# Kernel optimization log

Measured on AMD Instinct MI355X. Metric: run time of the kernel, lower is better.

The kernel has to match this reference:

```python
import jax, jax.numpy as jnp
import numpy as np

NUM_STEPS = 10
T0, T1 = 0.0, 1.0


def setup_inputs() -> dict:
    key = jax.random.key(0)
    ks = jax.random.split(key, 6)
    B, I, H = 4096, 1024, 2048
    sc_ih = 1.0 / np.sqrt(I)
    sc_hh = 1.0 / np.sqrt(H)
    return {
        "x": jax.random.normal(ks[0], (B, I), jnp.float32),
        "h0": jax.random.normal(ks[1], (B, H), jnp.float32),
        "W_ih": jax.random.normal(ks[2], (H, I), jnp.float32) * sc_ih,
        "b_ih": jax.random.normal(ks[3], (H,), jnp.float32) * sc_ih,
        "W_hh": jax.random.normal(ks[4], (H, H), jnp.float32) * sc_hh,
        "b_hh": jax.random.normal(ks[5], (H,), jnp.float32) * sc_hh,
        "tau": jnp.ones((H,), jnp.float32),
    }


def reference(x, h0, W_ih, b_ih, W_hh, b_hh, tau):
    dt = (T1 - T0) / NUM_STEPS
    # time-invariant input drive: W_ih(input) is the same every step
    ih = x @ W_ih.T + b_ih  # [B, H]
    decay = jnp.exp(-dt / tau)  # [H]

    def step(h, _):
        pre = ih + h @ W_hh.T + b_hh
        target = jnp.tanh(pre)
        h_new = decay * h + (1.0 - decay) * target
        return h_new, None

    h_final, _ = jax.lax.scan(step, h0, None, length=NUM_STEPS)
    return h_final
```

## Files before the change

### kernel.cpp

```cpp
#include <hip/hip_runtime.h>
#include <hip/hip_bf16.h>

#define NUM_STEPS 10
#define DT 0.1f

typedef __bf16 bf16_t;
typedef __bf16 bf16x8 __attribute__((ext_vector_type(8)));
typedef __bf16 bf16x4 __attribute__((ext_vector_type(4)));
typedef float f32x4 __attribute__((ext_vector_type(4)));

__device__ __forceinline__ void async16(const bf16_t* g, bf16_t* l) {
  __builtin_amdgcn_global_load_lds(
      (const __attribute__((address_space(1))) void*)g,
      (__attribute__((address_space(3))) void*)l, 16, 0, 0);
}

__global__ void cvt_f32_to_bf16(const float* __restrict__ in,
                                bf16_t* __restrict__ out, int n4) {
  int i = blockIdx.x * blockDim.x + threadIdx.x;
  if (i < n4) {
    float4 v = ((const float4*)in)[i];
    bf16x4 o = {(bf16_t)v.x, (bf16_t)v.y, (bf16_t)v.z, (bf16_t)v.w};
    ((bf16x4*)out)[i] = o;
  }
}

__global__ void make_decay(const float* __restrict__ tau,
                           float* __restrict__ decay, int n) {
  int i = blockIdx.x * blockDim.x + threadIdx.x;
  if (i < n) decay[i] = __expf(-DT / tau[i]);
}

template <int EPI>
__global__ __launch_bounds__(512, 2) void gemm_nt(
    const bf16_t* __restrict__ A, const bf16_t* __restrict__ Bw, int M, int N,
    int K, const float* __restrict__ bias1, const float* __restrict__ bias2,
    bf16_t* __restrict__ out_ihb, const bf16_t* __restrict__ ihb,
    const float* __restrict__ decay, const bf16_t* __restrict__ hb_prev,
    bf16_t* __restrict__ hb_next, float* __restrict__ out_f32, int writeOut) {
  extern __shared__ char smem[];

  const int tid = threadIdx.x;
  const int lane = tid & 63;
  const int wave = tid >> 6;
  const int waveM = wave >> 1;
  const int waveN = wave & 1;

  const int lin = blockIdx.y * gridDim.x + blockIdx.x;
  const int xcd = lin & 7;
  const int slot = lin >> 3;
  const int bx = (xcd & 1) * 8 + (slot & 7);
  const int by = (xcd >> 1) * 4 + (slot >> 3);
  const long bRow = (long)by * 256;
  const long bCol = (long)bx * 128;

  const int laneRow = lane & 15;
  const int laneK = (lane >> 4) << 3;
  const bf16_t* aG0 = A + (bRow + (wave * 2 + 0) * 16 + laneRow) * (long)K + laneK;
  const bf16_t* aG1 = A + (bRow + (wave * 2 + 1) * 16 + laneRow) * (long)K + laneK;
  const bf16_t* bG = Bw + (bCol + wave * 16 + laneRow) * (long)K + laneK;

  f32x4 acc[4][4] = {};

  auto stage = [&](int buf, int k0) {
    bf16_t* base = (bf16_t*)(smem + buf * 49152);
    async16(aG0 + k0, base + (wave * 2 + 0) * 1024);
    async16(aG0 + k0 + 32, base + (wave * 2 + 0) * 1024 + 512);
    async16(aG1 + k0, base + (wave * 2 + 1) * 1024);
    async16(aG1 + k0 + 32, base + (wave * 2 + 1) * 1024 + 512);
    async16(bG + k0, base + 16384 + wave * 1024);
    async16(bG + k0 + 32, base + 16384 + wave * 1024 + 512);
  };

  auto compute = [&](int buf) {
    const bf16_t* Ab = (const bf16_t*)(smem + buf * 49152);
    const bf16_t* Bb = Ab + 16384;
#pragma unroll
    for (int ks = 0; ks < 2; ++ks) {
      bf16x8 aF[4], bF[4];
#pragma unroll
      for (int t = 0; t < 4; ++t)
        aF[t] = *(const bf16x8*)&Ab[(waveM * 4 + t) * 1024 + ks * 512 + lane * 8];
#pragma unroll
      for (int u = 0; u < 4; ++u)
        bF[u] = *(const bf16x8*)&Bb[(waveN * 4 + u) * 1024 + ks * 512 + lane * 8];
      __builtin_amdgcn_s_setprio(1);
#pragma unroll
      for (int t = 0; t < 4; ++t)
#pragma unroll
        for (int u = 0; u < 4; ++u)
          acc[t][u] = __builtin_amdgcn_mfma_f32_16x16x32_bf16(aF[t], bF[u],
                                                              acc[t][u], 0, 0, 0);
      __builtin_amdgcn_s_setprio(0);
    }
  };

  const int NT = K >> 6;

  stage(0, 0);
  stage(1, 64);
  asm volatile("s_waitcnt vmcnt(6)" ::: "memory");
  __builtin_amdgcn_s_barrier();
  __builtin_amdgcn_sched_barrier(0);

  int cb = 0, sb = 2;
  for (int t = 0; t < NT - 2; ++t) {
    stage(sb, (t + 2) * 64);
    __builtin_amdgcn_sched_barrier(0);
    compute(cb);
    asm volatile("s_waitcnt lgkmcnt(0)" ::: "memory");
    asm volatile("s_waitcnt vmcnt(6)" ::: "memory");
    __builtin_amdgcn_s_barrier();
    __builtin_amdgcn_sched_barrier(0);
    cb = cb + 1; if (cb == 3) cb = 0;
    sb = sb + 1; if (sb == 3) sb = 0;
  }
  compute(cb);
  asm volatile("s_waitcnt lgkmcnt(0)" ::: "memory");
  asm volatile("s_waitcnt vmcnt(0)" ::: "memory");
  __builtin_amdgcn_s_barrier();
  __builtin_amdgcn_sched_barrier(0);
  cb = cb + 1; if (cb == 3) cb = 0;
  compute(cb);
  asm volatile("s_waitcnt lgkmcnt(0)" ::: "memory");
  __builtin_amdgcn_s_barrier();
  __builtin_amdgcn_sched_barrier(0);

  float* Ep = (float*)smem;
  const int eRow = (lane >> 4) << 2;
  const int eCol = lane & 15;
#pragma unroll
  for (int t = 0; t < 4; ++t)
#pragma unroll
    for (int u = 0; u < 4; ++u)
#pragma unroll
      for (int r = 0; r < 4; ++r) {
        const int rowL = waveM * 64 + t * 16 + eRow + r;
        const int colL = waveN * 64 + u * 16 + eCol;
        Ep[rowL * 128 + ((colL + 4 * rowL) & 127)] = acc[t][u][r];
      }
  asm volatile("s_waitcnt lgkmcnt(0)" ::: "memory");
  __builtin_amdgcn_s_barrier();
  __builtin_amdgcn_sched_barrier(0);

  const int rdRow = tid >> 3;
  const int col0 = (tid & 7) * 16;
#pragma unroll
  for (int p = 0; p < 4; ++p) {
    const int row = p * 64 + rdRow;
    float v[16];
#pragma unroll
    for (int c = 0; c < 4; ++c)
      *(f32x4*)&v[c * 4] =
          *(const f32x4*)&Ep[row * 128 + ((col0 + 4 * c + 4 * row) & 127)];
    const long g = (bRow + row) * (long)N + bCol + col0;

    if (EPI == 0) {
      f32x4 b1[4], b2[4];
#pragma unroll
      for (int c = 0; c < 4; ++c) {
        b1[c] = *(const f32x4*)&bias1[bCol + col0 + c * 4];
        b2[c] = *(const f32x4*)&bias2[bCol + col0 + c * 4];
      }
      bf16x8 o0, o1;
#pragma unroll
      for (int e = 0; e < 8; ++e)
        o0[e] = (bf16_t)(v[e] + b1[e >> 2][e & 3] + b2[e >> 2][e & 3]);
#pragma unroll
      for (int e = 0; e < 8; ++e)
        o1[e] = (bf16_t)(v[8 + e] + b1[2 + (e >> 2)][e & 3] +
                         b2[2 + (e >> 2)][e & 3]);
      *(bf16x8*)&out_ihb[g] = o0;
      *(bf16x8*)&out_ihb[g + 8] = o1;
    } else {
      const bf16x8 ih0 = *(const bf16x8*)&ihb[g];
      const bf16x8 ih1 = *(const bf16x8*)&ihb[g + 8];
      const bf16x8 hp0 = *(const bf16x8*)&hb_prev[g];
      const bf16x8 hp1 = *(const bf16x8*)&hb_prev[g + 8];
      f32x4 dc[4];
#pragma unroll
      for (int c = 0; c < 4; ++c)
        dc[c] = *(const f32x4*)&decay[bCol + col0 + c * 4];
      float hn[16];
      bf16x8 o0, o1;
#pragma unroll
      for (int e = 0; e < 8; ++e) {
        const float d = dc[e >> 2][e & 3];
        const float th = tanhf(v[e] + (float)ih0[e]);
        hn[e] = d * (float)hp0[e] + (1.0f - d) * th;
        o0[e] = (bf16_t)hn[e];
      }
#pragma unroll
      for (int e = 0; e < 8; ++e) {
        const float d = dc[2 + (e >> 2)][e & 3];
        const float th = tanhf(v[8 + e] + (float)ih1[e]);
        hn[8 + e] = d * (float)hp1[e] + (1.0f - d) * th;
        o1[e] = (bf16_t)hn[8 + e];
      }
      *(bf16x8*)&hb_next[g] = o0;
      *(bf16x8*)&hb_next[g + 8] = o1;
      if (writeOut) {
#pragma unroll
        for (int c = 0; c < 4; ++c)
          *(f32x4*)&out_f32[g + c * 4] = *(const f32x4*)&hn[c * 4];
      }
    }
  }
}

extern "C" void kernel_launch(void* const* d_in, const int* in_sizes, int n_in,
                              void* d_out, int out_size, void* d_ws,
                              size_t ws_size, hipStream_t stream) {
  const float* x = (const float*)d_in[0];
  const float* h0 = (const float*)d_in[1];
  const float* W_ih = (const float*)d_in[2];
  const float* b_ih = (const float*)d_in[3];
  const float* W_hh = (const float*)d_in[4];
  const float* b_hh = (const float*)d_in[5];
  const float* tau = (const float*)d_in[6];
  float* hout = (float*)d_out;

  const int B = 4096, I = 1024, H = 2048;

  char* ws = (char*)d_ws;
  bf16_t* ihb = (bf16_t*)ws; ws += (size_t)B * H * 2;
  bf16_t* hb0 = (bf16_t*)ws; ws += (size_t)B * H * 2;
  bf16_t* hb1 = (bf16_t*)ws; ws += (size_t)B * H * 2;
  bf16_t* xb = (bf16_t*)ws;  ws += (size_t)B * I * 2;
  bf16_t* wihb = (bf16_t*)ws; ws += (size_t)H * I * 2;
  bf16_t* whhb = (bf16_t*)ws; ws += (size_t)H * H * 2;
  float* decay = (float*)ws; ws += (size_t)H * 4;

  const int LDS_BYTES = 147456;
  (void)hipFuncSetAttribute(reinterpret_cast<const void*>(&gemm_nt<0>),
                            hipFuncAttributeMaxDynamicSharedMemorySize,
                            LDS_BYTES);
  (void)hipFuncSetAttribute(reinterpret_cast<const void*>(&gemm_nt<1>),
                            hipFuncAttributeMaxDynamicSharedMemorySize,
                            LDS_BYTES);

  cvt_f32_to_bf16<<<(B * I / 4 + 255) / 256, 256, 0, stream>>>(x, xb, B * I / 4);
  cvt_f32_to_bf16<<<(H * I / 4 + 255) / 256, 256, 0, stream>>>(W_ih, wihb, H * I / 4);
  cvt_f32_to_bf16<<<(H * H / 4 + 255) / 256, 256, 0, stream>>>(W_hh, whhb, H * H / 4);
  cvt_f32_to_bf16<<<(B * H / 4 + 255) / 256, 256, 0, stream>>>(h0, hb0, B * H / 4);
  make_decay<<<(H + 255) / 256, 256, 0, stream>>>(tau, decay, H);

  dim3 grid(H / 128, B / 256);
  gemm_nt<0><<<grid, 512, LDS_BYTES, stream>>>(
      xb, wihb, B, H, I, b_ih, b_hh, ihb, nullptr, nullptr, nullptr, nullptr,
      nullptr, 0);

  bf16_t* hb[2] = {hb0, hb1};
  for (int s = 0; s < NUM_STEPS; ++s) {
    gemm_nt<1><<<grid, 512, LDS_BYTES, stream>>>(
        hb[s & 1], whhb, B, H, H, nullptr, nullptr, nullptr, ihb, decay,
        hb[s & 1], hb[(s + 1) & 1], hout, (s == NUM_STEPS - 1) ? 1 : 0);
  }
}
```

Measured before the change: 735.9 us.

## Replace triple-buffered K pipeline with half-tile staged double buffering

Replaces the three-stage LDS ring with two buffers. Each 64-wide K tile is split into two 32-wide halves that are loaded and computed in alternating phases, so the next tile's halves are prefetched while the current halves are consumed. This shrinks the dynamic LDS request to the size the epilogue needs and aims to overlap global loads with MFMA work at a finer grain. In exchange it adds a second barrier per K tile and leaves less prefetch distance to hide memory latency.

```diff
diff --git a/kernel.cpp b/kernel.cpp
--- a/kernel.cpp
+++ b/kernel.cpp
@@ -62,69 +62,81 @@
 
   f32x4 acc[4][4] = {};
 
-  auto stage = [&](int buf, int k0) {
+  auto stage_h = [&](int buf, int k0, int ks) {
     bf16_t* base = (bf16_t*)(smem + buf * 49152);
-    async16(aG0 + k0, base + (wave * 2 + 0) * 1024);
-    async16(aG0 + k0 + 32, base + (wave * 2 + 0) * 1024 + 512);
-    async16(aG1 + k0, base + (wave * 2 + 1) * 1024);
-    async16(aG1 + k0 + 32, base + (wave * 2 + 1) * 1024 + 512);
-    async16(bG + k0, base + 16384 + wave * 1024);
-    async16(bG + k0 + 32, base + 16384 + wave * 1024 + 512);
+    const int ko = k0 + ks * 32;
+    async16(aG0 + ko, base + (wave * 2 + 0) * 1024 + ks * 512);
+    async16(aG1 + ko, base + (wave * 2 + 1) * 1024 + ks * 512);
+    async16(bG + ko, base + 16384 + wave * 1024 + ks * 512);
   };
 
-  auto compute = [&](int buf) {
+  auto phase_compute = [&](int buf, int ks) {
     const bf16_t* Ab = (const bf16_t*)(smem + buf * 49152);
     const bf16_t* Bb = Ab + 16384;
-#pragma unroll
-    for (int ks = 0; ks < 2; ++ks) {
-      bf16x8 aF[4], bF[4];
-#pragma unroll
-      for (int t = 0; t < 4; ++t)
-        aF[t] = *(const bf16x8*)&Ab[(waveM * 4 + t) * 1024 + ks * 512 + lane * 8];
+    bf16x8 aF[4], bF[4];
+#pragma unroll
+    for (int t = 0; t < 4; ++t)
+      aF[t] = *(const bf16x8*)&Ab[(waveM * 4 + t) * 1024 + ks * 512 + lane * 8];
+#pragma unroll
+    for (int u = 0; u < 4; ++u)
+      bF[u] = *(const bf16x8*)&Bb[(waveN * 4 + u) * 1024 + ks * 512 + lane * 8];
+    __builtin_amdgcn_s_setprio(1);
+#pragma unroll
+    for (int t = 0; t < 4; ++t)
 #pragma unroll
       for (int u = 0; u < 4; ++u)
-        bF[u] = *(const bf16x8*)&Bb[(waveN * 4 + u) * 1024 + ks * 512 + lane * 8];
-      __builtin_amdgcn_s_setprio(1);
-#pragma unroll
-      for (int t = 0; t < 4; ++t)
-#pragma unroll
-        for (int u = 0; u < 4; ++u)
-          acc[t][u] = __builtin_amdgcn_mfma_f32_16x16x32_bf16(aF[t], bF[u],
-                                                              acc[t][u], 0, 0, 0);
-      __builtin_amdgcn_s_setprio(0);
-    }
+        acc[t][u] = __builtin_amdgcn_mfma_f32_16x16x32_bf16(aF[t], bF[u],
+                                                            acc[t][u], 0, 0, 0);
+    __builtin_amdgcn_s_setprio(0);
   };
 
   const int NT = K >> 6;
 
-  stage(0, 0);
-  stage(1, 64);
+  stage_h(0, 0, 0);
+  stage_h(0, 0, 1);
+  stage_h(1, 64, 0);
   asm volatile("s_waitcnt vmcnt(6)" ::: "memory");
   __builtin_amdgcn_s_barrier();
   __builtin_amdgcn_sched_barrier(0);
 
-  int cb = 0, sb = 2;
+  int cur = 0;
   for (int t = 0; t < NT - 2; ++t) {
-    stage(sb, (t + 2) * 64);
-    __builtin_amdgcn_sched_barrier(0);
-    compute(cb);
+    const int k0 = t * 64;
+    stage_h(cur ^ 1, k0 + 64, 1);
+    phase_compute(cur, 0);
+    asm volatile("s_waitcnt vmcnt(6)" ::: "memory");
+    __builtin_amdgcn_s_barrier();
+    __builtin_amdgcn_sched_barrier(0);
+    stage_h(cur, k0 + 128, 0);
+    phase_compute(cur, 1);
+    asm volatile("s_waitcnt vmcnt(6)" ::: "memory");
+    __builtin_amdgcn_s_barrier();
+    __builtin_amdgcn_sched_barrier(0);
+    cur ^= 1;
+  }
+  {
+    const int k0 = (NT - 2) * 64;
+    stage_h(cur ^ 1, k0 + 64, 1);
+    phase_compute(cur, 0);
+    asm volatile("s_waitcnt vmcnt(6)" ::: "memory");
+    __builtin_amdgcn_s_barrier();
+    __builtin_amdgcn_sched_barrier(0);
+    phase_compute(cur, 1);
+    asm volatile("s_waitcnt vmcnt(3)" ::: "memory");
+    __builtin_amdgcn_s_barrier();
+    __builtin_amdgcn_sched_barrier(0);
+    cur ^= 1;
+  }
+  {
+    phase_compute(cur, 0);
+    asm volatile("s_waitcnt vmcnt(0)" ::: "memory");
+    __builtin_amdgcn_s_barrier();
+    __builtin_amdgcn_sched_barrier(0);
+    phase_compute(cur, 1);
     asm volatile("s_waitcnt lgkmcnt(0)" ::: "memory");
-    asm volatile("s_waitcnt vmcnt(6)" ::: "memory");
-    __builtin_amdgcn_s_barrier();
-    __builtin_amdgcn_sched_barrier(0);
-    cb = cb + 1; if (cb == 3) cb = 0;
-    sb = sb + 1; if (sb == 3) sb = 0;
-  }
-  compute(cb);
-  asm volatile("s_waitcnt lgkmcnt(0)" ::: "memory");
-  asm volatile("s_waitcnt vmcnt(0)" ::: "memory");
-  __builtin_amdgcn_s_barrier();
-  __builtin_amdgcn_sched_barrier(0);
-  cb = cb + 1; if (cb == 3) cb = 0;
-  compute(cb);
-  asm volatile("s_waitcnt lgkmcnt(0)" ::: "memory");
-  __builtin_amdgcn_s_barrier();
-  __builtin_amdgcn_sched_barrier(0);
+    __builtin_amdgcn_s_barrier();
+    __builtin_amdgcn_sched_barrier(0);
+  }
 
   float* Ep = (float*)smem;
   const int eRow = (lane >> 4) << 2;
@@ -231,7 +243,7 @@
   bf16_t* whhb = (bf16_t*)ws; ws += (size_t)H * H * 2;
   float* decay = (float*)ws; ws += (size_t)H * 4;
 
-  const int LDS_BYTES = 147456;
+  const int LDS_BYTES = 131072;
   (void)hipFuncSetAttribute(reinterpret_cast<const void*>(&gemm_nt<0>),
                             hipFuncAttributeMaxDynamicSharedMemorySize,
                             LDS_BYTES);
```

Result: no change. 736.7 us (+0.1%).

## Double GEMM block to 16 waves with smaller per-wave tiles

Applied to the files above, without the earlier changes.

Doubles the GEMM workgroup from 8 to 16 waves, so each wave owns a 64x32 output tile (4x2 MFMA accumulators) instead of 64x64, and the async global-to-LDS staging is spread across more waves. The per-k-step compute is split into two calls, and the lgkmcnt wait inside the main loop is removed. The aim is more waves in flight to hide memory latency, with lower register pressure per wave. The cost is smaller per-wave reuse: more LDS fragment reads per MFMA and barriers spanning 16 waves. Only one 1024-thread block fits per CU because of the LDS allocation, so the launch-bounds occupancy hint of 4 is not reachable.

```diff
diff --git a/kernel.cpp b/kernel.cpp
--- a/kernel.cpp
+++ b/kernel.cpp
@@ -32,7 +32,7 @@
 }
 
 template <int EPI>
-__global__ __launch_bounds__(512, 2) void gemm_nt(
+__global__ __launch_bounds__(1024, 4) void gemm_nt(
     const bf16_t* __restrict__ A, const bf16_t* __restrict__ Bw, int M, int N,
     int K, const float* __restrict__ bias1, const float* __restrict__ bias2,
     bf16_t* __restrict__ out_ihb, const bf16_t* __restrict__ ihb,
@@ -43,8 +43,8 @@
   const int tid = threadIdx.x;
   const int lane = tid & 63;
   const int wave = tid >> 6;
-  const int waveM = wave >> 1;
-  const int waveN = wave & 1;
+  const int waveM = wave >> 2;
+  const int waveN = wave & 3;
 
   const int lin = blockIdx.y * gridDim.x + blockIdx.x;
   const int xcd = lin & 7;
@@ -56,50 +56,46 @@
 
   const int laneRow = lane & 15;
   const int laneK = (lane >> 4) << 3;
-  const bf16_t* aG0 = A + (bRow + (wave * 2 + 0) * 16 + laneRow) * (long)K + laneK;
-  const bf16_t* aG1 = A + (bRow + (wave * 2 + 1) * 16 + laneRow) * (long)K + laneK;
-  const bf16_t* bG = Bw + (bCol + wave * 16 + laneRow) * (long)K + laneK;
-
-  f32x4 acc[4][4] = {};
+  const bf16_t* aG = A + (bRow + wave * 16 + laneRow) * (long)K + laneK;
+  const bf16_t* bG = Bw + (bCol + (wave & 7) * 16 + laneRow) * (long)K +
+                     laneK + (wave >> 3) * 32;
+  const int aOff = wave * 1024;
+  const int bOff = 16384 + (wave & 7) * 1024 + (wave >> 3) * 512;
+
+  f32x4 acc[4][2] = {};
 
   auto stage = [&](int buf, int k0) {
     bf16_t* base = (bf16_t*)(smem + buf * 49152);
-    async16(aG0 + k0, base + (wave * 2 + 0) * 1024);
-    async16(aG0 + k0 + 32, base + (wave * 2 + 0) * 1024 + 512);
-    async16(aG1 + k0, base + (wave * 2 + 1) * 1024);
-    async16(aG1 + k0 + 32, base + (wave * 2 + 1) * 1024 + 512);
-    async16(bG + k0, base + 16384 + wave * 1024);
-    async16(bG + k0 + 32, base + 16384 + wave * 1024 + 512);
+    async16(aG + k0, base + aOff);
+    async16(aG + k0 + 32, base + aOff + 512);
+    async16(bG + k0, base + bOff);
   };
 
-  auto compute = [&](int buf) {
+  auto compute = [&](int buf, int ks) {
     const bf16_t* Ab = (const bf16_t*)(smem + buf * 49152);
     const bf16_t* Bb = Ab + 16384;
-#pragma unroll
-    for (int ks = 0; ks < 2; ++ks) {
-      bf16x8 aF[4], bF[4];
-#pragma unroll
-      for (int t = 0; t < 4; ++t)
-        aF[t] = *(const bf16x8*)&Ab[(waveM * 4 + t) * 1024 + ks * 512 + lane * 8];
-#pragma unroll
-      for (int u = 0; u < 4; ++u)
-        bF[u] = *(const bf16x8*)&Bb[(waveN * 4 + u) * 1024 + ks * 512 + lane * 8];
-      __builtin_amdgcn_s_setprio(1);
-#pragma unroll
-      for (int t = 0; t < 4; ++t)
-#pragma unroll
-        for (int u = 0; u < 4; ++u)
-          acc[t][u] = __builtin_amdgcn_mfma_f32_16x16x32_bf16(aF[t], bF[u],
-                                                              acc[t][u], 0, 0, 0);
-      __builtin_amdgcn_s_setprio(0);
-    }
+    bf16x8 aF[4], bF[2];
+#pragma unroll
+    for (int t = 0; t < 4; ++t)
+      aF[t] = *(const bf16x8*)&Ab[(waveM * 4 + t) * 1024 + ks * 512 + lane * 8];
+#pragma unroll
+    for (int u = 0; u < 2; ++u)
+      bF[u] = *(const bf16x8*)&Bb[(waveN * 2 + u) * 1024 + ks * 512 + lane * 8];
+    __builtin_amdgcn_s_setprio(1);
+#pragma unroll
+    for (int t = 0; t < 4; ++t)
+#pragma unroll
+      for (int u = 0; u < 2; ++u)
+        acc[t][u] = __builtin_amdgcn_mfma_f32_16x16x32_bf16(aF[t], bF[u],
+                                                            acc[t][u], 0, 0, 0);
+    __builtin_amdgcn_s_setprio(0);
   };
 
   const int NT = K >> 6;
 
   stage(0, 0);
   stage(1, 64);
-  asm volatile("s_waitcnt vmcnt(6)" ::: "memory");
+  asm volatile("s_waitcnt vmcnt(3)" ::: "memory");
   __builtin_amdgcn_s_barrier();
   __builtin_amdgcn_sched_barrier(0);
 
@@ -107,21 +103,22 @@
   for (int t = 0; t < NT - 2; ++t) {
     stage(sb, (t + 2) * 64);
     __builtin_amdgcn_sched_barrier(0);
-    compute(cb);
-    asm volatile("s_waitcnt lgkmcnt(0)" ::: "memory");
-    asm volatile("s_waitcnt vmcnt(6)" ::: "memory");
+    compute(cb, 0);
+    compute(cb, 1);
+    asm volatile("s_waitcnt vmcnt(3)" ::: "memory");
     __builtin_amdgcn_s_barrier();
     __builtin_amdgcn_sched_barrier(0);
     cb = cb + 1; if (cb == 3) cb = 0;
     sb = sb + 1; if (sb == 3) sb = 0;
   }
-  compute(cb);
-  asm volatile("s_waitcnt lgkmcnt(0)" ::: "memory");
+  compute(cb, 0);
+  compute(cb, 1);
   asm volatile("s_waitcnt vmcnt(0)" ::: "memory");
   __builtin_amdgcn_s_barrier();
   __builtin_amdgcn_sched_barrier(0);
   cb = cb + 1; if (cb == 3) cb = 0;
-  compute(cb);
+  compute(cb, 0);
+  compute(cb, 1);
   asm volatile("s_waitcnt lgkmcnt(0)" ::: "memory");
   __builtin_amdgcn_s_barrier();
   __builtin_amdgcn_sched_barrier(0);
@@ -132,11 +129,11 @@
 #pragma unroll
   for (int t = 0; t < 4; ++t)
 #pragma unroll
-    for (int u = 0; u < 4; ++u)
+    for (int u = 0; u < 2; ++u)
 #pragma unroll
       for (int r = 0; r < 4; ++r) {
         const int rowL = waveM * 64 + t * 16 + eRow + r;
-        const int colL = waveN * 64 + u * 16 + eCol;
+        const int colL = waveN * 32 + u * 16 + eCol;
         Ep[rowL * 128 + ((colL + 4 * rowL) & 127)] = acc[t][u][r];
       }
   asm volatile("s_waitcnt lgkmcnt(0)" ::: "memory");
@@ -146,8 +143,8 @@
   const int rdRow = tid >> 3;
   const int col0 = (tid & 7) * 16;
 #pragma unroll
-  for (int p = 0; p < 4; ++p) {
-    const int row = p * 64 + rdRow;
+  for (int p = 0; p < 2; ++p) {
+    const int row = p * 128 + rdRow;
     float v[16];
 #pragma unroll
     for (int c = 0; c < 4; ++c)
@@ -246,13 +243,13 @@
   make_decay<<<(H + 255) / 256, 256, 0, stream>>>(tau, decay, H);
 
   dim3 grid(H / 128, B / 256);
-  gemm_nt<0><<<grid, 512, LDS_BYTES, stream>>>(
+  gemm_nt<0><<<grid, 1024, LDS_BYTES, stream>>>(
       xb, wihb, B, H, I, b_ih, b_hh, ihb, nullptr, nullptr, nullptr, nullptr,
       nullptr, 0);
 
   bf16_t* hb[2] = {hb0, hb1};
   for (int s = 0; s < NUM_STEPS; ++s) {
-    gemm_nt<1><<<grid, 512, LDS_BYTES, stream>>>(
+    gemm_nt<1><<<grid, 1024, LDS_BYTES, stream>>>(
         hb[s & 1], whhb, B, H, H, nullptr, nullptr, nullptr, ihb, decay,
         hb[s & 1], hb[(s + 1) & 1], hout, (s == NUM_STEPS - 1) ? 1 : 0);
   }
```

New measurement: 729.1 us. No clear change (-0.9%).

## Split k-tile into two half-phases interleaving A/B prefetch with MFMA clusters

Applied to the files above, without the earlier changes.

Restructures the GEMM main loop so each 64-wide k-tile is processed in two 32-wide phases. Each phase issues its LDS fragment reads, then half of the next tile's async global-to-LDS loads (A in one phase, B in the other), then a barrier and its MFMA cluster. The A tile staging layout also changes so each wave loads rows wave and wave+8 (lo/hi halves) instead of two adjacent 16-row blocks. The aim is to spread the global load issue through the loop and overlap it better with compute, at the cost of an extra barrier per tile.

```diff
diff --git a/kernel.cpp b/kernel.cpp
--- a/kernel.cpp
+++ b/kernel.cpp
@@ -3,6 +3,7 @@
 
 #define NUM_STEPS 10
 #define DT 0.1f
+#define SLOT_BYTES 49152
 
 typedef __bf16 bf16_t;
 typedef __bf16 bf16x8 __attribute__((ext_vector_type(8)));
@@ -48,96 +49,114 @@
 
   const int lin = blockIdx.y * gridDim.x + blockIdx.x;
   const int xcd = lin & 7;
-  const int slot = lin >> 3;
-  const int bx = (xcd & 1) * 8 + (slot & 7);
-  const int by = (xcd >> 1) * 4 + (slot >> 3);
+  const int slot_ = lin >> 3;
+  const int bx = (xcd & 1) * 8 + (slot_ & 7);
+  const int by = (xcd >> 1) * 4 + (slot_ >> 3);
   const long bRow = (long)by * 256;
   const long bCol = (long)bx * 128;
 
   const int laneRow = lane & 15;
   const int laneK = (lane >> 4) << 3;
-  const bf16_t* aG0 = A + (bRow + (wave * 2 + 0) * 16 + laneRow) * (long)K + laneK;
-  const bf16_t* aG1 = A + (bRow + (wave * 2 + 1) * 16 + laneRow) * (long)K + laneK;
+  const bf16_t* aGlo = A + (bRow + wave * 16 + laneRow) * (long)K + laneK;
+  const bf16_t* aGhi = A + (bRow + 128 + wave * 16 + laneRow) * (long)K + laneK;
   const bf16_t* bG = Bw + (bCol + wave * 16 + laneRow) * (long)K + laneK;
 
   f32x4 acc[4][4] = {};
 
-  auto stage = [&](int buf, int k0) {
-    bf16_t* base = (bf16_t*)(smem + buf * 49152);
-    async16(aG0 + k0, base + (wave * 2 + 0) * 1024);
-    async16(aG0 + k0 + 32, base + (wave * 2 + 0) * 1024 + 512);
-    async16(aG1 + k0, base + (wave * 2 + 1) * 1024);
-    async16(aG1 + k0 + 32, base + (wave * 2 + 1) * 1024 + 512);
+  auto stageA = [&](int slot, int k0) {
+    bf16_t* base = (bf16_t*)(smem + slot * SLOT_BYTES);
+    async16(aGlo + k0, base + wave * 1024);
+    async16(aGlo + k0 + 32, base + wave * 1024 + 512);
+    async16(aGhi + k0, base + (8 + wave) * 1024);
+    async16(aGhi + k0 + 32, base + (8 + wave) * 1024 + 512);
+  };
+  auto stageB = [&](int slot, int k0) {
+    bf16_t* base = (bf16_t*)(smem + slot * SLOT_BYTES);
     async16(bG + k0, base + 16384 + wave * 1024);
     async16(bG + k0 + 32, base + 16384 + wave * 1024 + 512);
   };
 
-  auto compute = [&](int buf) {
-    const bf16_t* Ab = (const bf16_t*)(smem + buf * 49152);
-    const bf16_t* Bb = Ab + 16384;
-#pragma unroll
-    for (int ks = 0; ks < 2; ++ks) {
-      bf16x8 aF[4], bF[4];
-#pragma unroll
-      for (int t = 0; t < 4; ++t)
-        aF[t] = *(const bf16x8*)&Ab[(waveM * 4 + t) * 1024 + ks * 512 + lane * 8];
-#pragma unroll
-      for (int u = 0; u < 4; ++u)
-        bF[u] = *(const bf16x8*)&Bb[(waveN * 4 + u) * 1024 + ks * 512 + lane * 8];
-      __builtin_amdgcn_s_setprio(1);
-#pragma unroll
-      for (int t = 0; t < 4; ++t)
-#pragma unroll
-        for (int u = 0; u < 4; ++u)
-          acc[t][u] = __builtin_amdgcn_mfma_f32_16x16x32_bf16(aF[t], bF[u],
-                                                              acc[t][u], 0, 0, 0);
-      __builtin_amdgcn_s_setprio(0);
-    }
-  };
-
   const int NT = K >> 6;
 
-  stage(0, 0);
-  stage(1, 64);
+  stageA(0, 0);
+  stageB(0, 0);
+  stageA(1, 64);
+  stageB(1, 64);
   asm volatile("s_waitcnt vmcnt(6)" ::: "memory");
   __builtin_amdgcn_s_barrier();
   __builtin_amdgcn_sched_barrier(0);
 
-  int cb = 0, sb = 2;
-  for (int t = 0; t < NT - 2; ++t) {
-    stage(sb, (t + 2) * 64);
-    __builtin_amdgcn_sched_barrier(0);
-    compute(cb);
-    asm volatile("s_waitcnt lgkmcnt(0)" ::: "memory");
-    asm volatile("s_waitcnt vmcnt(6)" ::: "memory");
-    __builtin_amdgcn_s_barrier();
-    __builtin_amdgcn_sched_barrier(0);
-    cb = cb + 1; if (cb == 3) cb = 0;
-    sb = sb + 1; if (sb == 3) sb = 0;
-  }
-  compute(cb);
-  asm volatile("s_waitcnt lgkmcnt(0)" ::: "memory");
-  asm volatile("s_waitcnt vmcnt(0)" ::: "memory");
-  __builtin_amdgcn_s_barrier();
-  __builtin_amdgcn_sched_barrier(0);
-  cb = cb + 1; if (cb == 3) cb = 0;
-  compute(cb);
-  asm volatile("s_waitcnt lgkmcnt(0)" ::: "memory");
-  __builtin_amdgcn_s_barrier();
-  __builtin_amdgcn_sched_barrier(0);
+  for (int t = 0; t < NT; ++t) {
+    const int slot = t % 3;
+    const int ns = (t + 2) % 3;
+    const int k2 = (t + 2) * 64;
+    const bool pf = (t + 2) < NT;
+    const bf16_t* Ab = (const bf16_t*)(smem + slot * SLOT_BYTES);
+    const bf16_t* Bb = Ab + 16384;
+
+    {
+      bf16x8 aF[4], bF[4];
+#pragma unroll
+      for (int i = 0; i < 4; ++i)
+        aF[i] = *(const bf16x8*)&Ab[(waveM * 4 + i) * 1024 + lane * 8];
+#pragma unroll
+      for (int u = 0; u < 4; ++u)
+        bF[u] = *(const bf16x8*)&Bb[(waveN * 4 + u) * 1024 + lane * 8];
+      if (pf) stageA(ns, k2);
+      __builtin_amdgcn_sched_barrier(0);
+      __builtin_amdgcn_s_barrier();
+      __builtin_amdgcn_s_setprio(1);
+#pragma unroll
+      for (int i = 0; i < 4; ++i)
+#pragma unroll
+        for (int u = 0; u < 4; ++u)
+          acc[i][u] = __builtin_amdgcn_mfma_f32_16x16x32_bf16(
+              aF[i], bF[u], acc[i][u], 0, 0, 0);
+      __builtin_amdgcn_s_setprio(0);
+      __builtin_amdgcn_sched_barrier(0);
+      __builtin_amdgcn_s_barrier();
+    }
+    {
+      bf16x8 aF[4], bF[4];
+#pragma unroll
+      for (int i = 0; i < 4; ++i)
+        aF[i] = *(const bf16x8*)&Ab[(waveM * 4 + i) * 1024 + 512 + lane * 8];
+#pragma unroll
+      for (int u = 0; u < 4; ++u)
+        bF[u] = *(const bf16x8*)&Bb[(waveN * 4 + u) * 1024 + 512 + lane * 8];
+      if (pf) stageB(ns, k2);
+      __builtin_amdgcn_sched_barrier(0);
+      __builtin_amdgcn_s_barrier();
+      __builtin_amdgcn_s_setprio(1);
+#pragma unroll
+      for (int i = 0; i < 4; ++i)
+#pragma unroll
+        for (int u = 0; u < 4; ++u)
+          acc[i][u] = __builtin_amdgcn_mfma_f32_16x16x32_bf16(
+              aF[i], bF[u], acc[i][u], 0, 0, 0);
+      __builtin_amdgcn_s_setprio(0);
+      if (t < NT - 2) {
+        asm volatile("s_waitcnt vmcnt(6)" ::: "memory");
+      } else if (t == NT - 2) {
+        asm volatile("s_waitcnt vmcnt(0)" ::: "memory");
+      }
+      __builtin_amdgcn_sched_barrier(0);
+      __builtin_amdgcn_s_barrier();
+    }
+  }
 
   float* Ep = (float*)smem;
   const int eRow = (lane >> 4) << 2;
   const int eCol = lane & 15;
 #pragma unroll
-  for (int t = 0; t < 4; ++t)
+  for (int i = 0; i < 4; ++i)
 #pragma unroll
     for (int u = 0; u < 4; ++u)
 #pragma unroll
       for (int r = 0; r < 4; ++r) {
-        const int rowL = waveM * 64 + t * 16 + eRow + r;
+        const int rowL = waveM * 64 + i * 16 + eRow + r;
         const int colL = waveN * 64 + u * 16 + eCol;
-        Ep[rowL * 128 + ((colL + 4 * rowL) & 127)] = acc[t][u][r];
+        Ep[rowL * 128 + ((colL + 4 * rowL) & 127)] = acc[i][u][r];
       }
   asm volatile("s_waitcnt lgkmcnt(0)" ::: "memory");
   __builtin_amdgcn_s_barrier();
```

After: 739.8 us. Within noise of the previous version (+0.5%).
